# Performance work log

Hardware: AMD Instinct MI355X
Metric: run time of the kernel (lower is better)

The kernel has to match this reference:

```python
import jax, jax.numpy as jnp
import numpy as np

N, E, B = 20000, 320000, 64
IN_DIM, HID, HEADS = 128, 64, 4
NEG_SLOPE = 0.2


def gat_conv(x, edge_index, W, a_src, a_dst, bias, concat):
    """PyG-style GATConv (eval mode, add_self_loops=True)."""
    n = x.shape[0]
    heads, C = a_src.shape
    loops = jnp.arange(n, dtype=edge_index.dtype)
    src = jnp.concatenate([edge_index[0], loops])
    dst = jnp.concatenate([edge_index[1], loops])
    h = (x @ W).reshape(n, heads, C)                      # [N,H,C]
    s_score = jnp.sum(h * a_src[None], axis=-1)           # [N,H]
    d_score = jnp.sum(h * a_dst[None], axis=-1)           # [N,H]
    e = jax.nn.leaky_relu(s_score[src] + d_score[dst], NEG_SLOPE)  # [E',H]
    m = jax.ops.segment_max(e, dst, num_segments=n)       # softmax over incoming edges
    ex = jnp.exp(e - m[dst])
    denom = jax.ops.segment_sum(ex, dst, num_segments=n)
    alpha = ex / (denom[dst] + 1e-16)                     # [E',H]
    out = jax.ops.segment_sum(h[src] * alpha[..., None], dst, num_segments=n)
    out = out.reshape(n, heads * C) if concat else out.mean(axis=1)
    return out + bias


def forward_graph(x, ei, batch, w1, as1, ad1, b1, w2, as2, ad2, b2, w3, as3, ad3, b3):
    x = jax.nn.elu(gat_conv(x, ei, w1, as1, ad1, b1, True))
    x = jax.nn.elu(gat_conv(x, ei, w2, as2, ad2, b2, True))
    x = jax.nn.elu(gat_conv(x, ei, w3, as3, ad3, b3, False))
    s = jax.ops.segment_sum(x, batch, num_segments=B)
    cnt = jax.ops.segment_sum(jnp.ones((x.shape[0],), x.dtype), batch, num_segments=B)
    return s / jnp.maximum(cnt, 1.0)[:, None]


def setup_inputs() -> dict:
    key = jax.random.key(0)
    ks = jax.random.split(key, 24)
    d = {}
    d['x_left'] = jax.random.normal(ks[0], (N, IN_DIM), jnp.float32)
    d['x_right'] = jax.random.normal(ks[1], (N, IN_DIM), jnp.float32)
    d['edge_index_left'] = jax.random.randint(ks[2], (2, E), 0, N, jnp.int32)
    d['edge_index_right'] = jax.random.randint(ks[3], (2, E), 0, N, jnp.int32)
    d['batch_left'] = jnp.sort(jax.random.randint(ks[4], (N,), 0, B, jnp.int32))
    d['batch_right'] = jnp.sort(jax.random.randint(ks[5], (N,), 0, B, jnp.int32))
    sc = 0.05
    d['w1'] = jax.random.normal(ks[6], (IN_DIM, HEADS * HID), jnp.float32) * sc
    d['as1'] = jax.random.normal(ks[7], (HEADS, HID), jnp.float32) * sc
    d['ad1'] = jax.random.normal(ks[8], (HEADS, HID), jnp.float32) * sc
    d['b1'] = jnp.zeros((HEADS * HID,), jnp.float32)
    d['w2'] = jax.random.normal(ks[9], (HEADS * HID, HEADS * HID), jnp.float32) * sc
    d['as2'] = jax.random.normal(ks[10], (HEADS, HID), jnp.float32) * sc
    d['ad2'] = jax.random.normal(ks[11], (HEADS, HID), jnp.float32) * sc
    d['b2'] = jnp.zeros((HEADS * HID,), jnp.float32)
    d['w3'] = jax.random.normal(ks[12], (HEADS * HID, HID), jnp.float32) * sc
    d['as3'] = jax.random.normal(ks[13], (1, HID), jnp.float32) * sc
    d['ad3'] = jax.random.normal(ks[14], (1, HID), jnp.float32) * sc
    d['b3'] = jnp.zeros((HID,), jnp.float32)
    d['fc1_w1'] = jax.random.normal(ks[15], (2 * HID, HID), jnp.float32) * sc
    d['fc1_b1'] = jnp.zeros((HID,), jnp.float32)
    d['fc1_w2'] = jax.random.normal(ks[16], (HID, 2), jnp.float32) * sc
    d['fc1_b2'] = jnp.zeros((2,), jnp.float32)
    d['fc2_w1'] = jax.random.normal(ks[17], (2 * HID, HID), jnp.float32) * sc
    d['fc2_b1'] = jnp.zeros((HID,), jnp.float32)
    d['fc2_w2'] = jax.random.normal(ks[18], (HID, 2), jnp.float32) * sc
    d['fc2_b2'] = jnp.zeros((2,), jnp.float32)
    return d


def reference(x_left, x_right, edge_index_left, edge_index_right, batch_left, batch_right,
              w1, as1, ad1, b1, w2, as2, ad2, b2, w3, as3, ad3, b3,
              fc1_w1, fc1_b1, fc1_w2, fc1_b2, fc2_w1, fc2_b1, fc2_w2, fc2_b2):
    gat = (w1, as1, ad1, b1, w2, as2, ad2, b2, w3, as3, ad3, b3)
    left = forward_graph(x_left, edge_index_left, batch_left, *gat)    # [B,HID]
    right = forward_graph(x_right, edge_index_right, batch_right, *gat)
    emb = jnp.concatenate([left, right], axis=1)                        # [B,2*HID]
    h1 = jax.nn.relu(emb @ fc1_w1 + fc1_b1)
    logits_hc_pd = h1 @ fc1_w2 + fc1_b2
    h2 = jax.nn.relu(emb @ fc2_w1 + fc2_b1)
    logits_pd_dd = h2 @ fc2_w2 + fc2_b2
    return logits_hc_pd, logits_pd_dd
```

## Files before the change

kernel.cpp:

```cpp
#include <hip/hip_runtime.h>
#include <cstdint>
#include <cstddef>

#define NNODES 20000
#define NEDGES 320000
#define NBATCH 64
#define EPRIME (NEDGES + NNODES)
#define SLOTS 64

typedef _Float16 half4 __attribute__((ext_vector_type(4)));
typedef _Float16 half8 __attribute__((ext_vector_type(8)));
typedef float floatx4 __attribute__((ext_vector_type(4)));


__global__ __launch_bounds__(256) void bucket_fill_kernel(const int* __restrict__ eiL,
                                                          const int* __restrict__ eiR,
                                                          int* __restrict__ cnt,
                                                          int* __restrict__ csr_src) {
    int k = blockIdx.x * 256 + threadIdx.x;
    if (k >= EPRIME) return;
    int side = blockIdx.y;
    const int* ei = side ? eiR : eiL;
    cnt     += side * NNODES;
    csr_src += (size_t)side * NNODES * SLOTS;
    int src, dst;
    if (k < NEDGES) { src = ei[k]; dst = ei[NEDGES + k]; }
    else            { src = k - NEDGES; dst = src; }
    int pos = atomicAdd(&cnt[dst], 1);
    if (pos < SLOTS) csr_src[dst * SLOTS + pos] = src;
}

__global__ __launch_bounds__(256) void bprep_kernel(const float* __restrict__ w1,
                                                    const float* __restrict__ w2,
                                                    const float* __restrict__ w3,
                                                    _Float16* __restrict__ bf) {
    int id = blockIdx.x * 256 + threadIdx.x;
    const float* B; int ngrp, Nn, base, off;
    if (id < 4096)       { B = w1; ngrp = 16; Nn = 256; base = 0;     off = 0; }
    else if (id < 12288) { B = w2; ngrp = 32; Nn = 256; base = 4096;  off = 32768; }
    else if (id < 14336) { B = w3; ngrp = 32; Nn = 64;  base = 12288; off = 98304; }
    else return;
    int tuple = id - base;
    int c  = tuple & 63;
    int kg = (tuple >> 6) % ngrp;
    int hd = (tuple >> 6) / ngrp;
    half8 hb;
#pragma unroll
    for (int j = 0; j < 8; j++)
        hb[j] = (_Float16)B[(size_t)(kg * 8 + j) * Nn + hd * 64 + c];
    *(half8*)&bf[(size_t)off + (size_t)tuple * 8] = hb;
}

__global__ __launch_bounds__(256) void mfma_sides_kernel(const float* __restrict__ AL,
                                                         const float* __restrict__ AR,
                                                         const _Float16* __restrict__ Bf,
                                                         _Float16* __restrict__ CL,
                                                         _Float16* __restrict__ CR,
                                                         int M, int K, int Nn,
                                                         const float* __restrict__ a_src,
                                                         const float* __restrict__ a_dst,
                                                         float* __restrict__ sL,
                                                         float* __restrict__ sR,
                                                         float* __restrict__ dL,
                                                         float* __restrict__ dR,
                                                         int H) {
    int side = blockIdx.z;
    const float* A = side ? AR : AL;
    _Float16* C = side ? CR : CL;
    float* s_sc = side ? sR : sL;
    float* d_sc = side ? dR : dL;

    __shared__ __align__(16) char smemA[2 * 128 * 40 * 2];
    auto Asl = (_Float16 (*)[128][40])smemA;

    int t = threadIdx.x;
    int w = t >> 6, lane = t & 63;
    int l4 = lane >> 4, l16 = lane & 15;
    int bm = blockIdx.x * 128;
    int head = blockIdx.y;
    int bn = head * 64;

    int ngrp = K >> 3;
    const _Float16* Bw = Bf + (size_t)head * ngrp * 512;

    int arow = t >> 1;
    int aks = (t & 1) * 16;
    bool arok = (bm + arow) < M;
    const float* Ap = A + (size_t)(arok ? (bm + arow) : (M - 1)) * K + aks;
    float4 ra0 = *(const float4*)&Ap[0];
    float4 ra1 = *(const float4*)&Ap[4];
    float4 ra2 = *(const float4*)&Ap[8];
    float4 ra3 = *(const float4*)&Ap[12];

    floatx4 acc[2][4] = {};

    int p = 0;
    for (int k0 = 0; k0 < K; k0 += 32, p ^= 1) {
        half8 h0, h1;
        h0[0] = (_Float16)ra0.x; h0[1] = (_Float16)ra0.y;
        h0[2] = (_Float16)ra0.z; h0[3] = (_Float16)ra0.w;
        h0[4] = (_Float16)ra1.x; h0[5] = (_Float16)ra1.y;
        h0[6] = (_Float16)ra1.z; h0[7] = (_Float16)ra1.w;
        h1[0] = (_Float16)ra2.x; h1[1] = (_Float16)ra2.y;
        h1[2] = (_Float16)ra2.z; h1[3] = (_Float16)ra2.w;
        h1[4] = (_Float16)ra3.x; h1[5] = (_Float16)ra3.y;
        h1[6] = (_Float16)ra3.z; h1[7] = (_Float16)ra3.w;
        *(half8*)&Asl[p][arow][aks]     = h0;
        *(half8*)&Asl[p][arow][aks + 8] = h1;
        int kn = k0 + 32;
        if (kn < K) {
            ra0 = *(const float4*)&Ap[kn + 0];
            ra1 = *(const float4*)&Ap[kn + 4];
            ra2 = *(const float4*)&Ap[kn + 8];
            ra3 = *(const float4*)&Ap[kn + 12];
        }
        int kg0 = (k0 >> 3) + l4;
        const _Float16* bp = &Bw[((kg0 << 6) + l16) * 8];
        half8 bf0 = *(const half8*)&bp[0];
        half8 bf1 = *(const half8*)&bp[16 * 8];
        half8 bf2 = *(const half8*)&bp[32 * 8];
        half8 bf3 = *(const half8*)&bp[48 * 8];
        __syncthreads();
        half8 af0 = *(const half8*)&Asl[p][w * 32 + l16][l4 * 8];
        half8 af1 = *(const half8*)&Asl[p][w * 32 + 16 + l16][l4 * 8];
        acc[0][0] = __builtin_amdgcn_mfma_f32_16x16x32_f16(af0, bf0, acc[0][0], 0, 0, 0);
        acc[1][0] = __builtin_amdgcn_mfma_f32_16x16x32_f16(af1, bf0, acc[1][0], 0, 0, 0);
        acc[0][1] = __builtin_amdgcn_mfma_f32_16x16x32_f16(af0, bf1, acc[0][1], 0, 0, 0);
        acc[1][1] = __builtin_amdgcn_mfma_f32_16x16x32_f16(af1, bf1, acc[1][1], 0, 0, 0);
        acc[0][2] = __builtin_amdgcn_mfma_f32_16x16x32_f16(af0, bf2, acc[0][2], 0, 0, 0);
        acc[1][2] = __builtin_amdgcn_mfma_f32_16x16x32_f16(af1, bf2, acc[1][2], 0, 0, 0);
        acc[0][3] = __builtin_amdgcn_mfma_f32_16x16x32_f16(af0, bf3, acc[0][3], 0, 0, 0);
        acc[1][3] = __builtin_amdgcn_mfma_f32_16x16x32_f16(af1, bf3, acc[1][3], 0, 0, 0);
    }

    float avv[4], dvv[4];
#pragma unroll
    for (int ni = 0; ni < 4; ni++) {
        avv[ni] = a_src[head * 64 + ni * 16 + l16];
        dvv[ni] = a_dst[head * 64 + ni * 16 + l16];
    }
#pragma unroll
    for (int mi = 0; mi < 2; mi++)
#pragma unroll
    for (int r = 0; r < 4; r++) {
        float ps = acc[mi][0][r] * avv[0] + acc[mi][1][r] * avv[1] +
                   acc[mi][2][r] * avv[2] + acc[mi][3][r] * avv[3];
        float pd = acc[mi][0][r] * dvv[0] + acc[mi][1][r] * dvv[1] +
                   acc[mi][2][r] * dvv[2] + acc[mi][3][r] * dvv[3];
#pragma unroll
        for (int off = 8; off >= 1; off >>= 1) {
            ps += __shfl_xor(ps, off);
            pd += __shfl_xor(pd, off);
        }
        int row = bm + w * 32 + mi * 16 + l4 * 4 + r;
        if (l16 == 0 && row < M) {
            s_sc[row * H + head] = ps;
            d_sc[row * H + head] = pd;
        }
    }

    __syncthreads();
    auto Cs = (_Float16 (*)[72])smemA;
#pragma unroll
    for (int mi = 0; mi < 2; mi++)
#pragma unroll
    for (int ni = 0; ni < 4; ni++)
#pragma unroll
    for (int r = 0; r < 4; r++)
        Cs[w * 32 + mi * 16 + l4 * 4 + r][ni * 16 + l16] = (_Float16)acc[mi][ni][r];
    __syncthreads();
    {
        int row = t >> 1, hh = t & 1;
        if (bm + row < M) {
            const half8* srcp = (const half8*)&Cs[row][hh * 32];
            half8 v0 = srcp[0], v1 = srcp[1], v2 = srcp[2], v3 = srcp[3];
            half8* dstp = (half8*)&C[(size_t)(bm + row) * Nn + bn + hh * 32];
            dstp[0] = v0; dstp[1] = v1; dstp[2] = v2; dstp[3] = v3;
        }
    }
}

template <int H, int C>
__global__ __launch_bounds__(256) void agg_kernel(const _Float16* __restrict__ hL,
                                                  const _Float16* __restrict__ hR,
                                                  const int* __restrict__ cntL,
                                                  const int* __restrict__ cntR,
                                                  const int* __restrict__ csL,
                                                  const int* __restrict__ csR,
                                                  const float* __restrict__ sL,
                                                  const float* __restrict__ sR,
                                                  const float* __restrict__ dL,
                                                  const float* __restrict__ dR,
                                                  const float* __restrict__ bias,
                                                  float* __restrict__ oL,
                                                  float* __restrict__ oR) {
    constexpr int HC = H * C;
    int side = blockIdx.y;
    const _Float16* hbuf = side ? hR   : hL;
    const int*   cnt     = side ? cntR : cntL;
    const int*   csr_src = side ? csR  : csL;
    const float* s_sc    = side ? sR   : sL;
    const float* d_sc    = side ? dR   : dL;
    float*       out     = side ? oR   : oL;

    __shared__ int   idxb[4][64];
    __shared__ __align__(16) float exb[4][64][H];
    int w = threadIdx.x >> 6, lane = threadIdx.x & 63;
    int n = blockIdx.x * 4 + w;
    if (n >= NNODES) return;
    int r0 = n * SLOTS;
    int deg = min(cnt[n], SLOTS);

    {
        int sl = 0;
        float exl[H];
#pragma unroll
        for (int h = 0; h < H; h++) exl[h] = 0.f;
        if (lane < deg) {
            sl = csr_src[r0 + lane];
#pragma unroll
            for (int h = 0; h < H; h++) {
                float e = s_sc[sl * H + h] + d_sc[n * H + h];
                e = (e >= 0.f) ? e : 0.2f * e;
                exl[h] = expf(e);
            }
        }
        idxb[w][lane] = sl * HC;
        if constexpr (H == 4) {
            *(float4*)&exb[w][lane][0] = make_float4(exl[0], exl[1], exl[2], exl[3]);
        } else {
            exb[w][lane][0] = exl[0];
        }
    }

    float acc[8] = {};
    float den = 0.f;

    if constexpr (H == 4) {
        int half = lane >> 5;
        int c32  = lane & 31;
        int hidx = c32 >> 3;
        const _Float16* hb = hbuf + c32 * 8;
        int steps = (deg + 1) >> 1;
        for (int s = 0; s < steps; s++) {
            int e = s * 2 + half;
            int idx = idxb[w][e];
            float ew = exb[w][e][hidx];
            half8 hv = *(const half8*)&hb[idx];
            den += ew;
#pragma unroll
            for (int k = 0; k < 8; k++) acc[k] += ew * (float)hv[k];
        }
        den += __shfl_xor(den, 32);
#pragma unroll
        for (int k = 0; k < 8; k++) acc[k] += __shfl_xor(acc[k], 32);
        float inv = 1.0f / (den + 1e-16f);
        int col = c32 * 8 + half * 4;
        float4 v;
#pragma unroll
        for (int k = 0; k < 4; k++) {
            float a = half ? acc[k + 4] : acc[k];
            float val = a * inv + bias[col + k];
            val = (val > 0.f) ? val : expm1f(val);
            (&v.x)[k] = val;
        }
        *(float4*)&out[(size_t)n * HC + col] = v;
    } else {
        int grp = lane >> 3;
        int c8  = lane & 7;
        const _Float16* hb = hbuf + c8 * 8;
        int steps = (deg + 7) >> 3;
        for (int s = 0; s < steps; s++) {
            int e = s * 8 + grp;
            int idx = idxb[w][e];
            float ew = exb[w][e][0];
            half8 hv = *(const half8*)&hb[idx];
            den += ew;
#pragma unroll
            for (int k = 0; k < 8; k++) acc[k] += ew * (float)hv[k];
        }
#pragma unroll
        for (int off = 8; off <= 32; off <<= 1) {
            den += __shfl_xor(den, off);
#pragma unroll
            for (int k = 0; k < 8; k++) acc[k] += __shfl_xor(acc[k], off);
        }
        if (lane < 16) {
            float inv = 1.0f / (den + 1e-16f);
            int sub = lane >> 3;
            int col = (lane & 7) * 8 + sub * 4;
            float4 v;
#pragma unroll
            for (int k = 0; k < 4; k++) {
                float a = sub ? acc[k + 4] : acc[k];
                float val = a * inv + bias[col + k];
                val = (val > 0.f) ? val : expm1f(val);
                (&v.x)[k] = val;
            }
            *(float4*)&out[(size_t)n * HC + col] = v;
        }
    }
}

__global__ __launch_bounds__(256) void pool_kernel(const float* __restrict__ xL,
                                                   const float* __restrict__ xR,
                                                   const int* __restrict__ baL,
                                                   const int* __restrict__ baR,
                                                   float* __restrict__ pL,
                                                   float* __restrict__ pR,
                                                   float* __restrict__ cL,
                                                   float* __restrict__ cR) {
    int side = blockIdx.y;
    const float* x     = side ? xR  : xL;
    const int*   batch = side ? baR : baL;
    float* pooled = side ? pR : pL;
    float* cntb   = side ? cR : cL;

    int b = blockIdx.x;
    int lo = 0, hi = NNODES;
    while (lo < hi) { int mid = (lo + hi) >> 1; if (batch[mid] < b) lo = mid + 1; else hi = mid; }
    int start = lo;
    hi = NNODES;
    while (lo < hi) { int mid = (lo + hi) >> 1; if (batch[mid] < b + 1) lo = mid + 1; else hi = mid; }
    int end = lo;

    int t = threadIdx.x;
    int c = t & 63, g = t >> 6;
    float s = 0.f;
    for (int n = start + g; n < end; n += 4) s += x[n * 64 + c];
    __shared__ float buf[4][64];
    buf[g][c] = s;
    __syncthreads();
    if (t < 64) {
        pooled[b * 64 + t] = buf[0][t] + buf[1][t] + buf[2][t] + buf[3][t];
        if (t == 0) cntb[b] = (float)(end - start);
    }
}

__global__ __launch_bounds__(256) void head_kernel(const float* __restrict__ pL,
                                                   const float* __restrict__ cL,
                                                   const float* __restrict__ pR,
                                                   const float* __restrict__ cR,
                                                   const float* __restrict__ w1a,
                                                   const float* __restrict__ b1a,
                                                   const float* __restrict__ w2a,
                                                   const float* __restrict__ b2a,
                                                   const float* __restrict__ w1b,
                                                   const float* __restrict__ b1b,
                                                   const float* __restrict__ w2b,
                                                   const float* __restrict__ b2b,
                                                   float* __restrict__ out) {
    int b = blockIdx.x;
    int t = threadIdx.x;
    __shared__ float emb[128];
    __shared__ float ph[4][64];
    __shared__ float h1[64];
    if (t < 64)        emb[t] = pL[b * 64 + t] / fmaxf(cL[b], 1.0f);
    else if (t < 128)  emb[t] = pR[b * 64 + (t - 64)] / fmaxf(cR[b], 1.0f);
    __syncthreads();
    int c = t & 63, g = t >> 6;
    {
        float p = 0.f;
#pragma unroll
        for (int k = 0; k < 32; k++) p += emb[g * 32 + k] * w1a[(g * 32 + k) * 64 + c];
        ph[g][c] = p;
        __syncthreads();
        if (t < 64) h1[t] = fmaxf(ph[0][t] + ph[1][t] + ph[2][t] + ph[3][t] + b1a[t], 0.f);
        __syncthreads();
        if (t < 128) {
            int o = t >> 6, lane = t & 63;
            float q = h1[lane] * w2a[lane * 2 + o];
#pragma unroll
            for (int off = 32; off >= 1; off >>= 1) q += __shfl_xor(q, off);
            if (lane == 0) out[b * 2 + o] = q + b2a[o];
        }
        __syncthreads();
    }
    {
        float p = 0.f;
#pragma unroll
        for (int k = 0; k < 32; k++) p += emb[g * 32 + k] * w1b[(g * 32 + k) * 64 + c];
        ph[g][c] = p;
        __syncthreads();
        if (t < 64) h1[t] = fmaxf(ph[0][t] + ph[1][t] + ph[2][t] + ph[3][t] + b1b[t], 0.f);
        __syncthreads();
        if (t < 128) {
            int o = t >> 6, lane = t & 63;
            float q = h1[lane] * w2b[lane * 2 + o];
#pragma unroll
            for (int off = 32; off >= 1; off >>= 1) q += __shfl_xor(q, off);
            if (lane == 0) out[128 + b * 2 + o] = q + b2b[o];
        }
    }
}

extern "C" void kernel_launch(void* const* d_in, const int* in_sizes, int n_in,
                              void* d_out, int out_size, void* d_ws, size_t ws_size,
                              hipStream_t stream) {
    const float* x_left   = (const float*)d_in[0];
    const float* x_right  = (const float*)d_in[1];
    const int*   ei_left  = (const int*)d_in[2];
    const int*   ei_right = (const int*)d_in[3];
    const int*   ba_left  = (const int*)d_in[4];
    const int*   ba_right = (const int*)d_in[5];
    const float* w1  = (const float*)d_in[6];
    const float* as1 = (const float*)d_in[7];
    const float* ad1 = (const float*)d_in[8];
    const float* b1  = (const float*)d_in[9];
    const float* w2  = (const float*)d_in[10];
    const float* as2 = (const float*)d_in[11];
    const float* ad2 = (const float*)d_in[12];
    const float* b2  = (const float*)d_in[13];
    const float* w3  = (const float*)d_in[14];
    const float* as3 = (const float*)d_in[15];
    const float* ad3 = (const float*)d_in[16];
    const float* b3  = (const float*)d_in[17];
    const float* f1w1 = (const float*)d_in[18];
    const float* f1b1 = (const float*)d_in[19];
    const float* f1w2 = (const float*)d_in[20];
    const float* f1b2 = (const float*)d_in[21];
    const float* f2w1 = (const float*)d_in[22];
    const float* f2b1 = (const float*)d_in[23];
    const float* f2w2 = (const float*)d_in[24];
    const float* f2b2 = (const float*)d_in[25];

    const size_t NEED = (size_t)95 * 1024 * 1024;
    int ns = (ws_size >= NEED) ? 2 : 1;

    char* w = (char*)d_ws;
    auto carve = [&](size_t bytes) {
        void* p = (void*)w;
        w += (bytes + 255) & ~(size_t)255;
        return p;
    };
    const size_t HSTR = (size_t)NNODES * 256;
    _Float16* hbf  = (_Float16*)carve((size_t)ns * HSTR * 2);
    float* buf1    = (float*)carve((size_t)ns * HSTR * 4);
    float* s_sc    = (float*)carve((size_t)ns * NNODES * 4 * 4);
    float* d_sc    = (float*)carve((size_t)ns * NNODES * 4 * 4);
    int*   cnt     = (int*)carve((size_t)ns * NNODES * 4);
    int*   csr     = (int*)carve((size_t)ns * NNODES * SLOTS * 4);
    float* pooled  = (float*)carve(2 * 64 * 64 * 4);
    float* cntb    = (float*)carve(2 * 64 * 4);
    _Float16* bfw  = (_Float16*)carve(114688 * 2);

    _Float16* bf1 = bfw;
    _Float16* bf2 = bfw + 32768;
    _Float16* bf3 = bfw + 98304;

    const int egrid  = (EPRIME + 255) / 256;
    const int ngrid  = (NNODES + 3) / 4;
    const int mgrid2 = (NNODES + 127) / 128;

    if (ns == 2) {
        _Float16* h_L = hbf;          _Float16* h_R = hbf + HSTR;
        float* o_L = buf1;            float* o_R = buf1 + HSTR;
        float* sL = s_sc;             float* sR = s_sc + NNODES * 4;
        float* dL = d_sc;             float* dR = d_sc + NNODES * 4;
        int* cnL = cnt;               int* cnR = cnt + NNODES;
        int* csL = csr;               int* csR = csr + (size_t)NNODES * SLOTS;

        hipMemsetAsync(cnt, 0, (size_t)2 * NNODES * 4, stream);
        bprep_kernel<<<56, 256, 0, stream>>>(w1, w2, w3, bfw);
        bucket_fill_kernel<<<dim3(egrid, 2), 256, 0, stream>>>(ei_left, ei_right, cnt, csr);

        mfma_sides_kernel<<<dim3(mgrid2, 4, 2), 256, 0, stream>>>(
            x_left, x_right, bf1, h_L, h_R, NNODES, 128, 256, as1, ad1, sL, sR, dL, dR, 4);
        agg_kernel<4, 64><<<dim3(ngrid, 2), 256, 0, stream>>>(
            h_L, h_R, cnL, cnR, csL, csR, sL, sR, dL, dR, b1, o_L, o_R);
        mfma_sides_kernel<<<dim3(mgrid2, 4, 2), 256, 0, stream>>>(
            o_L, o_R, bf2, h_L, h_R, NNODES, 256, 256, as2, ad2, sL, sR, dL, dR, 4);
        agg_kernel<4, 64><<<dim3(ngrid, 2), 256, 0, stream>>>(
            h_L, h_R, cnL, cnR, csL, csR, sL, sR, dL, dR, b2, o_L, o_R);
        mfma_sides_kernel<<<dim3(mgrid2, 1, 2), 256, 0, stream>>>(
            o_L, o_R, bf3, h_L, h_R, NNODES, 256, 64, as3, ad3, sL, sR, dL, dR, 1);
        agg_kernel<1, 64><<<dim3(ngrid, 2), 256, 0, stream>>>(
            h_L, h_R, cnL, cnR, csL, csR, sL, sR, dL, dR, b3, o_L, o_R);

        pool_kernel<<<dim3(NBATCH, 2), 256, 0, stream>>>(
            o_L, o_R, ba_left, ba_right, pooled, pooled + 4096, cntb, cntb + 64);
        head_kernel<<<NBATCH, 256, 0, stream>>>(pooled, cntb, pooled + 4096, cntb + 64,
                                                f1w1, f1b1, f1w2, f1b2,
                                                f2w1, f2b1, f2w2, f2b2,
                                                (float*)d_out);
    } else {
        bprep_kernel<<<56, 256, 0, stream>>>(w1, w2, w3, bfw);
        for (int side = 0; side < 2; side++) {
            const float* x_in  = side ? x_right  : x_left;
            const int*   ei    = side ? ei_right : ei_left;
            const int*   batch = side ? ba_right : ba_left;
            float* pside = pooled + side * 4096;
            float* cside = cntb + side * 64;

            hipMemsetAsync(cnt, 0, (size_t)NNODES * 4, stream);
            bucket_fill_kernel<<<dim3(egrid, 1), 256, 0, stream>>>(ei, ei, cnt, csr);

            mfma_sides_kernel<<<dim3(mgrid2, 4, 1), 256, 0, stream>>>(
                x_in, x_in, bf1, hbf, hbf, NNODES, 128, 256, as1, ad1, s_sc, s_sc, d_sc, d_sc, 4);
            agg_kernel<4, 64><<<dim3(ngrid, 1), 256, 0, stream>>>(
                hbf, hbf, cnt, cnt, csr, csr, s_sc, s_sc, d_sc, d_sc, b1, buf1, buf1);

            mfma_sides_kernel<<<dim3(mgrid2, 4, 1), 256, 0, stream>>>(
                buf1, buf1, bf2, hbf, hbf, NNODES, 256, 256, as2, ad2, s_sc, s_sc, d_sc, d_sc, 4);
            agg_kernel<4, 64><<<dim3(ngrid, 1), 256, 0, stream>>>(
                hbf, hbf, cnt, cnt, csr, csr, s_sc, s_sc, d_sc, d_sc, b2, buf1, buf1);

            mfma_sides_kernel<<<dim3(mgrid2, 1, 1), 256, 0, stream>>>(
                buf1, buf1, bf3, hbf, hbf, NNODES, 256, 64, as3, ad3, s_sc, s_sc, d_sc, d_sc, 1);
            agg_kernel<1, 64><<<dim3(ngrid, 1), 256, 0, stream>>>(
                hbf, hbf, cnt, cnt, csr, csr, s_sc, s_sc, d_sc, d_sc, b3, buf1, buf1);

            pool_kernel<<<dim3(NBATCH, 1), 256, 0, stream>>>(
                buf1, buf1, batch, batch, pside, pside, cside, cside);
        }
        head_kernel<<<NBATCH, 256, 0, stream>>>(pooled, cntb, pooled + 4096, cntb + 64,
                                                f1w1, f1b1, f1w2, f1b2,
                                                f2w1, f2b1, f2w2, f2b2,
                                                (float*)d_out);
    }
}
```

Before: 394.3 us.

## Add 64-row all-heads MFMA GEMM kernel and unroll aggregation gather loops

Adds a new GEMM kernel for layers 1 and 2. Each block covers 64 rows and all 4 heads, one wave per head, with double-buffered fp16 A tiles in shared memory and an LDS-staged coalesced output write. The A tile is loaded and converted once per block instead of once per head-block, and the attention scores are computed in the epilogue. Separately, the aggregation gather loops are unrolled by 4 with independent loads to raise memory-level parallelism. The cost is more registers for the 64 accumulators and a smaller grid in the GEMM kernel.

```diff
diff --git a/kernel.cpp b/kernel.cpp
--- a/kernel.cpp
+++ b/kernel.cpp
@@ -49,6 +49,135 @@
     for (int j = 0; j < 8; j++)
         hb[j] = (_Float16)B[(size_t)(kg * 8 + j) * Nn + hd * 64 + c];
     *(half8*)&bf[(size_t)off + (size_t)tuple * 8] = hb;
+}
+
+__global__ __launch_bounds__(256) void mfma_heads_kernel(const float* __restrict__ AL,
+                                                         const float* __restrict__ AR,
+                                                         const _Float16* __restrict__ Bf,
+                                                         _Float16* __restrict__ CL,
+                                                         _Float16* __restrict__ CR,
+                                                         int M, int K,
+                                                         const float* __restrict__ a_src,
+                                                         const float* __restrict__ a_dst,
+                                                         float* __restrict__ sL,
+                                                         float* __restrict__ sR,
+                                                         float* __restrict__ dL,
+                                                         float* __restrict__ dR) {
+    int side = blockIdx.z;
+    const float* A = side ? AR : AL;
+    _Float16* C = side ? CR : CL;
+    float* s_sc = side ? sR : sL;
+    float* d_sc = side ? dR : dL;
+
+    __shared__ __align__(16) char smem[64 * 288 * 2];
+    auto Asl = (_Float16 (*)[64][40])smem;
+
+    int t = threadIdx.x;
+    int w = t >> 6, lane = t & 63;
+    int l4 = lane >> 4, l16 = lane & 15;
+    int bm = blockIdx.x * 64;
+
+    int ngrp = K >> 3;
+    const _Float16* Bw = Bf + (size_t)w * ngrp * 512;
+
+    int arow = t >> 2;
+    int aks = (t & 3) * 8;
+    bool arok = (bm + arow) < M;
+    const float* Ap = A + (size_t)(arok ? (bm + arow) : (M - 1)) * K + aks;
+    float4 ra0 = *(const float4*)&Ap[0];
+    float4 ra1 = *(const float4*)&Ap[4];
+
+    floatx4 acc[4][4] = {};
+
+    int p = 0;
+    for (int k0 = 0; k0 < K; k0 += 32, p ^= 1) {
+        half8 h0;
+        h0[0] = (_Float16)ra0.x; h0[1] = (_Float16)ra0.y;
+        h0[2] = (_Float16)ra0.z; h0[3] = (_Float16)ra0.w;
+        h0[4] = (_Float16)ra1.x; h0[5] = (_Float16)ra1.y;
+        h0[6] = (_Float16)ra1.z; h0[7] = (_Float16)ra1.w;
+        *(half8*)&Asl[p][arow][aks] = h0;
+        int kn = k0 + 32;
+        if (kn < K) {
+            ra0 = *(const float4*)&Ap[kn + 0];
+            ra1 = *(const float4*)&Ap[kn + 4];
+        }
+        int kg0 = (k0 >> 3) + l4;
+        const _Float16* bp = &Bw[((kg0 << 6) + l16) * 8];
+        half8 bf0 = *(const half8*)&bp[0];
+        half8 bf1 = *(const half8*)&bp[16 * 8];
+        half8 bf2 = *(const half8*)&bp[32 * 8];
+        half8 bf3 = *(const half8*)&bp[48 * 8];
+        __syncthreads();
+        half8 af0 = *(const half8*)&Asl[p][l16][l4 * 8];
+        half8 af1 = *(const half8*)&Asl[p][16 + l16][l4 * 8];
+        half8 af2 = *(const half8*)&Asl[p][32 + l16][l4 * 8];
+        half8 af3 = *(const half8*)&Asl[p][48 + l16][l4 * 8];
+        acc[0][0] = __builtin_amdgcn_mfma_f32_16x16x32_f16(af0, bf0, acc[0][0], 0, 0, 0);
+        acc[1][0] = __builtin_amdgcn_mfma_f32_16x16x32_f16(af1, bf0, acc[1][0], 0, 0, 0);
+        acc[2][0] = __builtin_amdgcn_mfma_f32_16x16x32_f16(af2, bf0, acc[2][0], 0, 0, 0);
+        acc[3][0] = __builtin_amdgcn_mfma_f32_16x16x32_f16(af3, bf0, acc[3][0], 0, 0, 0);
+        acc[0][1] = __builtin_amdgcn_mfma_f32_16x16x32_f16(af0, bf1, acc[0][1], 0, 0, 0);
+        acc[1][1] = __builtin_amdgcn_mfma_f32_16x16x32_f16(af1, bf1, acc[1][1], 0, 0, 0);
+        acc[2][1] = __builtin_amdgcn_mfma_f32_16x16x32_f16(af2, bf1, acc[2][1], 0, 0, 0);
+        acc[3][1] = __builtin_amdgcn_mfma_f32_16x16x32_f16(af3, bf1, acc[3][1], 0, 0, 0);
+        acc[0][2] = __builtin_amdgcn_mfma_f32_16x16x32_f16(af0, bf2, acc[0][2], 0, 0, 0);
+        acc[1][2] = __builtin_amdgcn_mfma_f32_16x16x32_f16(af1, bf2, acc[1][2], 0, 0, 0);
+        acc[2][2] = __builtin_amdgcn_mfma_f32_16x16x32_f16(af2, bf2, acc[2][2], 0, 0, 0);
+        acc[3][2] = __builtin_amdgcn_mfma_f32_16x16x32_f16(af3, bf2, acc[3][2], 0, 0, 0);
+        acc[0][3] = __builtin_amdgcn_mfma_f32_16x16x32_f16(af0, bf3, acc[0][3], 0, 0, 0);
+        acc[1][3] = __builtin_amdgcn_mfma_f32_16x16x32_f16(af1, bf3, acc[1][3], 0, 0, 0);
+        acc[2][3] = __builtin_amdgcn_mfma_f32_16x16x32_f16(af2, bf3, acc[2][3], 0, 0, 0);
+        acc[3][3] = __builtin_amdgcn_mfma_f32_16x16x32_f16(af3, bf3, acc[3][3], 0, 0, 0);
+    }
+
+    float avv[4], dvv[4];
+#pragma unroll
+    for (int ni = 0; ni < 4; ni++) {
+        avv[ni] = a_src[w * 64 + ni * 16 + l16];
+        dvv[ni] = a_dst[w * 64 + ni * 16 + l16];
+    }
+#pragma unroll
+    for (int mi = 0; mi < 4; mi++)
+#pragma unroll
+    for (int r = 0; r < 4; r++) {
+        float ps = acc[mi][0][r] * avv[0] + acc[mi][1][r] * avv[1] +
+                   acc[mi][2][r] * avv[2] + acc[mi][3][r] * avv[3];
+        float pd = acc[mi][0][r] * dvv[0] + acc[mi][1][r] * dvv[1] +
+                   acc[mi][2][r] * dvv[2] + acc[mi][3][r] * dvv[3];
+#pragma unroll
+        for (int off = 8; off >= 1; off >>= 1) {
+            ps += __shfl_xor(ps, off);
+            pd += __shfl_xor(pd, off);
+        }
+        int row = bm + mi * 16 + l4 * 4 + r;
+        if (l16 == 0 && row < M) {
+            s_sc[row * 4 + w] = ps;
+            d_sc[row * 4 + w] = pd;
+        }
+    }
+
+    __syncthreads();
+    auto Cs = (_Float16 (*)[288])smem;
+#pragma unroll
+    for (int mi = 0; mi < 4; mi++)
+#pragma unroll
+    for (int ni = 0; ni < 4; ni++)
+#pragma unroll
+    for (int r = 0; r < 4; r++)
+        Cs[mi * 16 + l4 * 4 + r][w * 72 + ni * 16 + l16] = (_Float16)acc[mi][ni][r];
+    __syncthreads();
+    {
+        int row = t >> 2, q = t & 3;
+        if (bm + row < M) {
+            const half8* sp = (const half8*)&Cs[row][q * 72];
+            half8 v0 = sp[0], v1 = sp[1], v2 = sp[2], v3 = sp[3];
+            half8 v4 = sp[4], v5 = sp[5], v6 = sp[6], v7 = sp[7];
+            half8* dp = (half8*)&C[(size_t)(bm + row) * 256 + q * 64];
+            dp[0] = v0; dp[1] = v1; dp[2] = v2; dp[3] = v3;
+            dp[4] = v4; dp[5] = v5; dp[6] = v6; dp[7] = v7;
+        }
+    }
 }
 
 __global__ __launch_bounds__(256) void mfma_sides_kernel(const float* __restrict__ AL,
@@ -237,47 +366,85 @@
     float den = 0.f;
 
     if constexpr (H == 4) {
-        int half = lane >> 5;
-        int c32  = lane & 31;
+        int hf  = lane >> 5;
+        int c32 = lane & 31;
         int hidx = c32 >> 3;
         const _Float16* hb = hbuf + c32 * 8;
         int steps = (deg + 1) >> 1;
-        for (int s = 0; s < steps; s++) {
-            int e = s * 2 + half;
-            int idx = idxb[w][e];
-            float ew = exb[w][e][hidx];
-            half8 hv = *(const half8*)&hb[idx];
-            den += ew;
-#pragma unroll
-            for (int k = 0; k < 8; k++) acc[k] += ew * (float)hv[k];
+        int sb = steps & ~3;
+        int s = 0;
+        for (; s < sb; s += 4) {
+            int e = 2 * s + hf;
+            int i0 = idxb[w][e],     i1 = idxb[w][e + 2];
+            int i2 = idxb[w][e + 4], i3 = idxb[w][e + 6];
+            float w0 = exb[w][e][hidx],     w1 = exb[w][e + 2][hidx];
+            float w2 = exb[w][e + 4][hidx], w3 = exb[w][e + 6][hidx];
+            half8 v0 = *(const half8*)&hb[i0];
+            half8 v1 = *(const half8*)&hb[i1];
+            half8 v2 = *(const half8*)&hb[i2];
+            half8 v3 = *(const half8*)&hb[i3];
+            den += (w0 + w1) + (w2 + w3);
+#pragma unroll
+            for (int k = 0; k < 8; k++)
+                acc[k] += w0 * (float)v0[k] + w1 * (float)v1[k] +
+                          w2 * (float)v2[k] + w3 * (float)v3[k];
+        }
+        for (; s < steps; s++) {
+            int e = 2 * s + hf;
+            int i0 = idxb[w][e];
+            float w0 = exb[w][e][hidx];
+            half8 v0 = *(const half8*)&hb[i0];
+            den += w0;
+#pragma unroll
+            for (int k = 0; k < 8; k++) acc[k] += w0 * (float)v0[k];
         }
         den += __shfl_xor(den, 32);
 #pragma unroll
         for (int k = 0; k < 8; k++) acc[k] += __shfl_xor(acc[k], 32);
         float inv = 1.0f / (den + 1e-16f);
-        int col = c32 * 8 + half * 4;
+        int col = c32 * 8 + hf * 4;
         float4 v;
-#pragma unroll
-        for (int k = 0; k < 4; k++) {
-            float a = half ? acc[k + 4] : acc[k];
-            float val = a * inv + bias[col + k];
-            val = (val > 0.f) ? val : expm1f(val);
-            (&v.x)[k] = val;
-        }
+        float b0 = bias[col + 0], b1 = bias[col + 1], b2 = bias[col + 2], b3 = bias[col + 3];
+        float a0 = hf ? acc[4] : acc[0];
+        float a1 = hf ? acc[5] : acc[1];
+        float a2 = hf ? acc[6] : acc[2];
+        float a3 = hf ? acc[7] : acc[3];
+        v.x = a0 * inv + b0; v.x = (v.x > 0.f) ? v.x : expm1f(v.x);
+        v.y = a1 * inv + b1; v.y = (v.y > 0.f) ? v.y : expm1f(v.y);
+        v.z = a2 * inv + b2; v.z = (v.z > 0.f) ? v.z : expm1f(v.z);
+        v.w = a3 * inv + b3; v.w = (v.w > 0.f) ? v.w : expm1f(v.w);
         *(float4*)&out[(size_t)n * HC + col] = v;
     } else {
         int grp = lane >> 3;
         int c8  = lane & 7;
         const _Float16* hb = hbuf + c8 * 8;
         int steps = (deg + 7) >> 3;
-        for (int s = 0; s < steps; s++) {
+        int sb = steps & ~3;
+        int s = 0;
+        for (; s < sb; s += 4) {
             int e = s * 8 + grp;
-            int idx = idxb[w][e];
-            float ew = exb[w][e][0];
-            half8 hv = *(const half8*)&hb[idx];
-            den += ew;
-#pragma unroll
-            for (int k = 0; k < 8; k++) acc[k] += ew * (float)hv[k];
+            int i0 = idxb[w][e],      i1 = idxb[w][e + 8];
+            int i2 = idxb[w][e + 16], i3 = idxb[w][e + 24];
+            float w0 = exb[w][e][0],      w1 = exb[w][e + 8][0];
+            float w2 = exb[w][e + 16][0], w3 = exb[w][e + 24][0];
+            half8 v0 = *(const half8*)&hb[i0];
+            half8 v1 = *(const half8*)&hb[i1];
+            half8 v2 = *(const half8*)&hb[i2];
+            half8 v3 = *(const half8*)&hb[i3];
+            den += (w0 + w1) + (w2 + w3);
+#pragma unroll
+            for (int k = 0; k < 8; k++)
+                acc[k] += w0 * (float)v0[k] + w1 * (float)v1[k] +
+                          w2 * (float)v2[k] + w3 * (float)v3[k];
+        }
+        for (; s < steps; s++) {
+            int e = s * 8 + grp;
+            int i0 = idxb[w][e];
+            float w0 = exb[w][e][0];
+            half8 v0 = *(const half8*)&hb[i0];
+            den += w0;
+#pragma unroll
+            for (int k = 0; k < 8; k++) acc[k] += w0 * (float)v0[k];
         }
 #pragma unroll
         for (int off = 8; off <= 32; off <<= 1) {
@@ -290,13 +457,14 @@
             int sub = lane >> 3;
             int col = (lane & 7) * 8 + sub * 4;
             float4 v;
-#pragma unroll
-            for (int k = 0; k < 4; k++) {
-                float a = sub ? acc[k + 4] : acc[k];
-                float val = a * inv + bias[col + k];
-                val = (val > 0.f) ? val : expm1f(val);
-                (&v.x)[k] = val;
-            }
+            float a0 = sub ? acc[4] : acc[0];
+            float a1 = sub ? acc[5] : acc[1];
+            float a2 = sub ? acc[6] : acc[2];
+            float a3 = sub ? acc[7] : acc[3];
+            v.x = a0 * inv + bias[col + 0]; v.x = (v.x > 0.f) ? v.x : expm1f(v.x);
+            v.y = a1 * inv + bias[col + 1]; v.y = (v.y > 0.f) ? v.y : expm1f(v.y);
+            v.z = a2 * inv + bias[col + 2]; v.z = (v.z > 0.f) ? v.z : expm1f(v.z);
+            v.w = a3 * inv + bias[col + 3]; v.w = (v.w > 0.f) ? v.w : expm1f(v.w);
             *(float4*)&out[(size_t)n * HC + col] = v;
         }
     }
@@ -450,7 +618,8 @@
 
     const int egrid  = (EPRIME + 255) / 256;
     const int ngrid  = (NNODES + 3) / 4;
-    const int mgrid2 = (NNODES + 127) / 128;
+    const int mgrid64  = (NNODES + 63) / 64;
+    const int mgrid128 = (NNODES + 127) / 128;
 
     if (ns == 2) {
         _Float16* h_L = hbf;          _Float16* h_R = hbf + HSTR;
@@ -464,15 +633,15 @@
         bprep_kernel<<<56, 256, 0, stream>>>(w1, w2, w3, bfw);
         bucket_fill_kernel<<<dim3(egrid, 2), 256, 0, stream>>>(ei_left, ei_right, cnt, csr);
 
-        mfma_sides_kernel<<<dim3(mgrid2, 4, 2), 256, 0, stream>>>(
-            x_left, x_right, bf1, h_L, h_R, NNODES, 128, 256, as1, ad1, sL, sR, dL, dR, 4);
+        mfma_heads_kernel<<<dim3(mgrid64, 1, 2), 256, 0, stream>>>(
+            x_left, x_right, bf1, h_L, h_R, NNODES, 128, as1, ad1, sL, sR, dL, dR);
         agg_kernel<4, 64><<<dim3(ngrid, 2), 256, 0, stream>>>(
             h_L, h_R, cnL, cnR, csL, csR, sL, sR, dL, dR, b1, o_L, o_R);
-        mfma_sides_kernel<<<dim3(mgrid2, 4, 2), 256, 0, stream>>>(
-            o_L, o_R, bf2, h_L, h_R, NNODES, 256, 256, as2, ad2, sL, sR, dL, dR, 4);
+        mfma_heads_kernel<<<dim3(mgrid64, 1, 2), 256, 0, stream>>>(
+            o_L, o_R, bf2, h_L, h_R, NNODES, 256, as2, ad2, sL, sR, dL, dR);
         agg_kernel<4, 64><<<dim3(ngrid, 2), 256, 0, stream>>>(
             h_L, h_R, cnL, cnR, csL, csR, sL, sR, dL, dR, b2, o_L, o_R);
-        mfma_sides_kernel<<<dim3(mgrid2, 1, 2), 256, 0, stream>>>(
+        mfma_sides_kernel<<<dim3(mgrid128, 1, 2), 256, 0, stream>>>(
             o_L, o_R, bf3, h_L, h_R, NNODES, 256, 64, as3, ad3, sL, sR, dL, dR, 1);
         agg_kernel<1, 64><<<dim3(ngrid, 2), 256, 0, stream>>>(
             h_L, h_R, cnL, cnR, csL, csR, sL, sR, dL, dR, b3, o_L, o_R);
@@ -495,17 +664,17 @@
             hipMemsetAsync(cnt, 0, (size_t)NNODES * 4, stream);
             bucket_fill_kernel<<<dim3(egrid, 1), 256, 0, stream>>>(ei, ei, cnt, csr);
 
-            mfma_sides_kernel<<<dim3(mgrid2, 4, 1), 256, 0, stream>>>(
-                x_in, x_in, bf1, hbf, hbf, NNODES, 128, 256, as1, ad1, s_sc, s_sc, d_sc, d_sc, 4);
+            mfma_heads_kernel<<<dim3(mgrid64, 1, 1), 256, 0, stream>>>(
+                x_in, x_in, bf1, hbf, hbf, NNODES, 128, as1, ad1, s_sc, s_sc, d_sc, d_sc);
             agg_kernel<4, 64><<<dim3(ngrid, 1), 256, 0, stream>>>(
                 hbf, hbf, cnt, cnt, csr, csr, s_sc, s_sc, d_sc, d_sc, b1, buf1, buf1);
 
-            mfma_sides_kernel<<<dim3(mgrid2, 4, 1), 256, 0, stream>>>(
-                buf1, buf1, bf2, hbf, hbf, NNODES, 256, 256, as2, ad2, s_sc, s_sc, d_sc, d_sc, 4);
+            mfma_heads_kernel<<<dim3(mgrid64, 1, 1), 256, 0, stream>>>(
+                buf1, buf1, bf2, hbf, hbf, NNODES, 256, as2, ad2, s_sc, s_sc, d_sc, d_sc);
             agg_kernel<4, 64><<<dim3(ngrid, 1), 256, 0, stream>>>(
                 hbf, hbf, cnt, cnt, csr, csr, s_sc, s_sc, d_sc, d_sc, b2, buf1, buf1);
 
-            mfma_sides_kernel<<<dim3(mgrid2, 1, 1), 256, 0, stream>>>(
+            mfma_sides_kernel<<<dim3(mgrid128, 1, 1), 256, 0, stream>>>(
                 buf1, buf1, bf3, hbf, hbf, NNODES, 256, 64, as3, ad3, s_sc, s_sc, d_sc, d_sc, 1);
             agg_kernel<1, 64><<<dim3(ngrid, 1), 256, 0, stream>>>(
                 hbf, hbf, cnt, cnt, csr, csr, s_sc, s_sc, d_sc, d_sc, b3, buf1, buf1);
```

After: 350.2 us. 11.2% less time.
